# Performance work log

Measured on AMD Instinct MI355X. Metric: run time of the kernel, lower is better.

Reference implementation:

```python
import jax, jax.numpy as jnp
import numpy as np

LAYERS = 3
N_NODES = 100000
N_EDGES = 800000
EMB = 100
EPS = 1e-12  # F.normalize default eps


def setup_inputs() -> dict:
    key = jax.random.key(0)
    ks = jax.random.split(key, 7)
    embedding = jax.random.normal(ks[0], (N_NODES, EMB), dtype=jnp.float32)
    adj_val = jax.random.uniform(ks[1], (N_EDGES,), dtype=jnp.float32)
    w_att = jax.random.normal(ks[2], (EMB, 1), dtype=jnp.float32) * 0.1
    b_att = jax.random.normal(ks[3], (1,), dtype=jnp.float32) * 0.1
    w_items = jax.random.normal(ks[4], (LAYERS, EMB, EMB), dtype=jnp.float32) * 0.1
    adj_row = jax.random.randint(ks[5], (N_EDGES,), 0, N_NODES, dtype=jnp.int32)
    adj_col = jax.random.randint(ks[6], (N_EDGES,), 0, N_NODES, dtype=jnp.int32)
    return {"embedding": embedding, "adj_val": adj_val, "w_att": w_att,
            "b_att": b_att, "w_items": w_items, "adj_row": adj_row, "adj_col": adj_col}


def reference(embedding, adj_val, w_att, b_att, w_items, adj_row, adj_col):
    n = embedding.shape[0]
    # column-degree normalization: adjacency.multiply(1/adjacency.sum(axis=0))
    degree = jax.ops.segment_sum(adj_val, adj_col, num_segments=n)  # [N]
    vals = adj_val / degree[adj_col]  # per-edge normalized value

    x = embedding
    final = embedding
    for i in range(LAYERS):
        scores = x @ w_att + b_att              # [N,1]
        attw = jax.nn.softmax(scores, axis=0)   # softmax over nodes (dim=0)
        x = x @ w_items[i].T                    # nn.Linear (no bias)
        m = x * attw                            # attention-weighted features
        # sparse mm: out[r] = sum_{edges e: row[e]=r} vals[e] * m[col[e]]
        gathered = m[adj_col] * vals[:, None]   # [E, EMB]
        x = jax.ops.segment_sum(gathered, adj_row, num_segments=n)
        # F.normalize(p=2, dim=-1)
        norm = jnp.linalg.norm(x, axis=-1, keepdims=True)
        x = x / jnp.maximum(norm, EPS)
        final = final + x
    return final / (LAYERS + 1)
```

## Files before the change

### kernel.cpp

```cpp
#include <hip/hip_runtime.h>
#include <hip/hip_bf16.h>

#define NN 100000
#define NE 800000
#define EM 100
#define NL 3

typedef short bf16x8 __attribute__((ext_vector_type(8)));
typedef float f32x4  __attribute__((ext_vector_type(4)));
typedef unsigned long long u64;

static constexpr size_t OFF_XB   = 0;
static constexpr size_t OFF_M    = OFF_XB   + (size_t)NN*128*2;
static constexpr size_t OFF_F    = OFF_M    + (size_t)NN*128;
static constexpr size_t OFF_DEG  = OFF_F    + (size_t)NN*EM*2;
static constexpr size_t OFF_SC   = OFF_DEG  + (size_t)NN*4;
static constexpr size_t OFF_ES   = OFF_SC   + (size_t)NN*4;
static constexpr size_t OFF_POS  = OFF_ES   + (size_t)NE*8;
static constexpr size_t OFF_CNT  = OFF_POS  + (size_t)NE*4;
static constexpr size_t OFF_RP   = OFF_CNT  + (size_t)NN*4;
static constexpr size_t OFF_DGF  = OFF_RP   + (size_t)(NN+64)*4;
static constexpr size_t OFF_BS   = OFF_DGF  + (size_t)NN*8;
static constexpr size_t OFF_BIN  = OFF_BS   + 512;
static constexpr size_t OFF_FLAG = OFF_BIN  + 32768;
static constexpr size_t OFF_WAT  = OFF_FLAG + 16;
static constexpr size_t OFF_WBF  = OFF_WAT  + 512;

#define DEG_SCALE  4294967296.0f
#define DEG_INV    (1.0f/4294967296.0f)
#define BIN_SCALE  1048576.0f
#define BIN_INV    (1.0f/1048576.0f)

__device__ inline float ldf(const void* p, int i, int f32) {
    return f32 ? ((const float*)p)[i]
               : __bfloat162float(((const __hip_bfloat16*)p)[i]);
}

__device__ inline float bflo(unsigned int u) { return __uint_as_float(u << 16); }
__device__ inline float bfhi(unsigned int u) { return __uint_as_float(u & 0xFFFF0000u); }
__device__ inline unsigned int pack2bf(float a, float b) {
    __hip_bfloat16 ha = __float2bfloat16(a), hb = __float2bfloat16(b);
    unsigned short ua = *(unsigned short*)&ha, ub = *(unsigned short*)&hb;
    return (unsigned int)ua | ((unsigned int)ub << 16);
}
__device__ inline float ub0(unsigned int x) { return (float)(x & 0xFF); }
__device__ inline float ub1(unsigned int x) { return (float)((x >> 8) & 0xFF); }
__device__ inline float ub2(unsigned int x) { return (float)((x >> 16) & 0xFF); }
__device__ inline float ub3(unsigned int x) { return (float)(x >> 24); }

__device__ inline int probe_block(const void* p, int nsamp) {
    __shared__ int sflag;
    int tid = threadIdx.x;
    if (tid < 64) {
        const unsigned short* h = (const unsigned short*)p;
        int big = 0;
        for (int i = tid; i < nsamp; i += 64) {
            int ex = (h[2 * i] >> 7) & 0xFF;
            big += (ex >= 134) ? 1 : 0;
        }
        #pragma unroll
        for (int off = 32; off; off >>= 1) big += __shfl_xor(big, off);
        if (tid == 0) sflag = (big >= 2) ? 1 : 0;
    }
    __syncthreads();
    int f = sflag;
    __syncthreads();
    return f;
}

__global__ __launch_bounds__(256) void k_setup(const void* w_att, const void* w_itm,
                                               u64* degfix, int* counts, u64* bins,
                                               float* wat, unsigned short* wbf) {
    int fw = probe_block(w_att, 50);
    int fi = probe_block(w_itm, 256);
    int i = blockIdx.x * 256 + threadIdx.x;
    if (i < NN) { degfix[i] = 0ull; counts[i] = 0; }
    if (i < 4096) bins[i] = 0ull;
    if (i < 128) wat[i] = (i < EM) ? ldf(w_att, i, fw) : 0.f;
    if (i < NL * 112 * 128) {
        int l = i / (112 * 128), rem = i % (112 * 128);
        int n = rem >> 7, k = rem & 127;
        float v = (n < EM && k < EM) ? ldf(w_itm, (l * EM + n) * EM + k, fi) : 0.f;
        __hip_bfloat16 b = __float2bfloat16(v);
        wbf[i] = *(unsigned short*)&b;
    }
}

__global__ __launch_bounds__(256) void k_initxf(const void* __restrict__ emb,
                                                const float* __restrict__ wat,
                                                unsigned int* __restrict__ xbf,
                                                unsigned int* __restrict__ fin,
                                                float* __restrict__ scores, int* flags,
                                                u64* __restrict__ bins) {
    __shared__ float sb[4];
    int femb = probe_block(emb, 256);
    if (blockIdx.x == 0 && threadIdx.x == 0) flags[0] = femb;
    int lane = threadIdx.x & 63, w = threadIdx.x >> 6;
    int r = blockIdx.x * 4 + w;
    float f0 = 0.f, f1 = 0.f, part = 0.f;
    bool act = lane < 50;
    if (act) {
        if (femb) {
            float2 t = ((const float2*)emb)[(size_t)r * 50 + lane];
            f0 = t.x; f1 = t.y;
        } else {
            unsigned int u = ((const unsigned int*)emb)[(size_t)r * 50 + lane];
            f0 = bflo(u); f1 = bfhi(u);
        }
        float2 wv = *(const float2*)(wat + 2 * lane);
        part = f0 * wv.x + f1 * wv.y;
        fin[(size_t)r * 50 + lane] = pack2bf(f0, f1);
    }
    xbf[(size_t)r * 64 + lane] = act ? pack2bf(f0, f1) : 0u;
    #pragma unroll
    for (int off = 32; off; off >>= 1) part += __shfl_xor(part, off);
    if (lane == 0) {
        float p = expf(part);
        scores[r] = p;
        sb[w] = p;
    }
    __syncthreads();
    if (threadIdx.x == 0) {
        float t = sb[0] + sb[1] + sb[2] + sb[3];
        atomicAdd(&bins[blockIdx.x & 1023], (u64)llrintf(t * BIN_SCALE));
    }
}

__global__ __launch_bounds__(256) void k_deg(const void* __restrict__ val,
                                             const int* __restrict__ row, const int* __restrict__ col,
                                             u64* degfix, int* counts, int* __restrict__ pos) {
    int fav = probe_block(val, 256);
    int e = blockIdx.x * 256 + threadIdx.x;
    if (e >= NE) return;
    float v = ldf(val, e, fav);
    atomicAdd(&degfix[col[e]], (u64)llrintf(v * DEG_SCALE));
    pos[e] = atomicAdd(&counts[row[e]], 1);
}

__global__ __launch_bounds__(256) void k_scanA(const int* __restrict__ counts, int* excl, int* bsum,
                                               const u64* __restrict__ degfix, float* __restrict__ deg) {
    __shared__ int s[256];
    int base = blockIdx.x * 1024;
    int tid = threadIdx.x;
    int v[4]; int t = 0;
    #pragma unroll
    for (int i = 0; i < 4; i++) {
        int idx = base + tid * 4 + i;
        v[i] = (idx < NN) ? counts[idx] : 0;
        if (idx < NN) deg[idx] = (float)degfix[idx] * DEG_INV;
        t += v[i];
    }
    s[tid] = t; __syncthreads();
    for (int off = 1; off < 256; off <<= 1) {
        int add = (tid >= off) ? s[tid - off] : 0;
        __syncthreads();
        s[tid] += add;
        __syncthreads();
    }
    int ex = (tid == 0) ? 0 : s[tid - 1];
    #pragma unroll
    for (int i = 0; i < 4; i++) {
        int idx = base + tid * 4 + i;
        if (idx < NN) excl[idx] = ex;
        ex += v[i];
    }
    if (tid == 255) bsum[blockIdx.x] = s[255];
}

__global__ __launch_bounds__(256) void k_scanC(int* rowptr, const int* __restrict__ bsum) {
    __shared__ int spfx;
    int tid = threadIdx.x;
    int gi = blockIdx.x >> 2;
    if (tid < 64) {
        int t = (tid < gi) ? bsum[tid] : 0;
        if (tid + 64 < gi) t += bsum[tid + 64];
        #pragma unroll
        for (int off = 32; off; off >>= 1) t += __shfl_xor(t, off);
        if (tid == 0) spfx = t;
    }
    __syncthreads();
    int pfx = spfx;
    int i = blockIdx.x * 256 + tid;
    if (i < NN) {
        rowptr[i] += pfx;
        if (i == 0) rowptr[NN] = NE;
    }
}

__global__ __launch_bounds__(256) void k_scatter(const int* __restrict__ row, const int* __restrict__ col,
                                                 const void* __restrict__ aval,
                                                 const int* __restrict__ rowptr,
                                                 const int* __restrict__ pos, int2* es) {
    int fav = probe_block(aval, 256);
    int e = blockIdx.x * 256 + threadIdx.x;
    if (e >= NE) return;
    int p = rowptr[row[e]] + pos[e];
    es[p] = make_int2(col[e], __float_as_int(ldf(aval, e, fav)));
}

__global__ __launch_bounds__(256) void k_gemm(const unsigned short* __restrict__ xbf,
                                              const unsigned short* __restrict__ wbf,
                                              const float* __restrict__ scores,
                                              const u64* __restrict__ bins,
                                              const float* __restrict__ deg,
                                              unsigned char* __restrict__ m, int layer) {
    int wid = threadIdx.x >> 6, lane = threadIdx.x & 63;
    int row0 = blockIdx.x * 64 + wid * 16;
    if (row0 >= NN) return;
    int c15 = lane & 15, quad = lane >> 4;

    u64 bs = 0;
    const u64* bp = bins + (size_t)layer * 1024;
    #pragma unroll
    for (int t = 0; t < 16; t++) bs += bp[t * 64 + lane];
    #pragma unroll
    for (int off = 32; off; off >>= 1) bs += __shfl_xor(bs, off);
    float inv_sum = 1.0f / ((float)bs * BIN_INV);

    const bf16x8* xa = (const bf16x8*)(xbf + (size_t)(row0 + c15) * 128 + quad * 8);
    bf16x8 a[4];
    #pragma unroll
    for (int kq = 0; kq < 4; kq++) a[kq] = xa[kq * 4];

    float att[4];
    #pragma unroll
    for (int r = 0; r < 4; r++) {
        int grow = row0 + quad * 4 + r;
        float dv = deg[grow];
        float invd = dv > 0.f ? 1.0f / dv : 0.f;
        att[r] = scores[grow] * inv_sum * invd;
    }

    const bf16x8* wb = (const bf16x8*)(wbf + (size_t)layer * 112 * 128
                                       + (size_t)c15 * 128 + quad * 8);
    f32x4 accs[7];
    #pragma unroll
    for (int nt = 0; nt < 7; nt++) {
        f32x4 acc = {0.f, 0.f, 0.f, 0.f};
        #pragma unroll
        for (int kq = 0; kq < 4; kq++) {
            bf16x8 b = wb[nt * 256 + kq * 4];
            acc = __builtin_amdgcn_mfma_f32_16x16x32_bf16(a[kq], b, acc, 0, 0, 0);
        }
        accs[nt] = acc;
    }
    #pragma unroll
    for (int r = 0; r < 4; r++) {
        float mx = 0.f;
        #pragma unroll
        for (int nt = 0; nt < 7; nt++) mx = fmaxf(mx, fabsf(accs[nt][r]));
        #pragma unroll
        for (int off = 1; off < 16; off <<= 1) mx = fmaxf(mx, __shfl_xor(mx, off));
        float inv = 127.0f / fmaxf(mx, 1e-30f);
        int grow = row0 + quad * 4 + r;
        unsigned char* rowp = m + (size_t)grow * 128;
        #pragma unroll
        for (int nt = 0; nt < 7; nt++) {
            int col = nt * 16 + c15;
            if (col < EM) {
                int q = (int)rintf(accs[nt][r] * inv) + 128;
                rowp[col] = (unsigned char)q;
            }
        }
        if (c15 == 0) *(float*)(rowp + 100) = att[r] * mx * (1.0f / 127.0f);
        if (c15 < 6)  *(unsigned int*)(rowp + 104 + 4 * c15) = 0x80808080u;
    }
}

__global__ __launch_bounds__(256) void k_spmm(const int* __restrict__ rowptr,
                                              const int2* __restrict__ es,
                                              const unsigned char* __restrict__ m,
                                              const float* __restrict__ wat,
                                              unsigned int* __restrict__ xbf,
                                              unsigned int* __restrict__ fin,
                                              float* __restrict__ scores,
                                              void* __restrict__ out, const int* flags,
                                              u64* __restrict__ bins,
                                              int layer, int last) {
    __shared__ float sb[4];
    int lane = threadIdx.x & 63;
    int w = threadIdx.x >> 6;
    int r = blockIdx.x * 4 + w;
    int slot = lane >> 4, k = lane & 15;
    int s = rowptr[r], e = rowptr[r + 1];
    const char* mq = (const char*)m;
    int src12 = (lane & 48) + 12;

    float acc[8] = {0.f, 0.f, 0.f, 0.f, 0.f, 0.f, 0.f, 0.f};
    float tsum = 0.f;
    for (int i = s; i < e; i += 8) {
        int i0 = i + slot, i1 = i + 4 + slot;
        int j0 = i0 < e - 1 ? i0 : e - 1;
        int j1 = i1 < e - 1 ? i1 : e - 1;
        int2 c0 = es[j0];
        int2 c1 = es[j1];
        float v0 = (i0 < e) ? __int_as_float(c0.y) : 0.f;
        float v1 = (i1 < e) ? __int_as_float(c1.y) : 0.f;
        uint2 u0 = *(const uint2*)(mq + (((size_t)c0.x) << 7) + (k << 3));
        uint2 u1 = *(const uint2*)(mq + (((size_t)c1.x) << 7) + (k << 3));
        float s0 = __uint_as_float(__shfl((int)u0.y, src12));
        float s1 = __uint_as_float(__shfl((int)u1.y, src12));
        float t0 = v0 * s0, t1 = v1 * s1;
        tsum += t0 + t1;
        unsigned int x0 = u0.x, y0 = (k == 12) ? 0x80808080u : u0.y;
        unsigned int x1 = u1.x, y1 = (k == 12) ? 0x80808080u : u1.y;
        acc[0] += t0 * ub0(x0); acc[1] += t0 * ub1(x0);
        acc[2] += t0 * ub2(x0); acc[3] += t0 * ub3(x0);
        acc[4] += t0 * ub0(y0); acc[5] += t0 * ub1(y0);
        acc[6] += t0 * ub2(y0); acc[7] += t0 * ub3(y0);
        acc[0] += t1 * ub0(x1); acc[1] += t1 * ub1(x1);
        acc[2] += t1 * ub2(x1); acc[3] += t1 * ub3(x1);
        acc[4] += t1 * ub0(y1); acc[5] += t1 * ub1(y1);
        acc[6] += t1 * ub2(y1); acc[7] += t1 * ub3(y1);
    }
    #pragma unroll
    for (int t = 0; t < 8; t++) {
        acc[t] += __shfl_xor(acc[t], 16);
        acc[t] += __shfl_xor(acc[t], 32);
    }
    tsum += __shfl_xor(tsum, 16);
    tsum += __shfl_xor(tsum, 32);
    float corr = 128.0f * tsum;
    #pragma unroll
    for (int t = 0; t < 8; t++) acc[t] -= corr;

    float sq = 0.f;
    #pragma unroll
    for (int t = 0; t < 8; t++) sq += acc[t] * acc[t];
    #pragma unroll
    for (int off = 8; off; off >>= 1) sq += __shfl_xor(sq, off);
    float rn = 1.f / fmaxf(sqrtf(sq), 1e-12f);
    float n[8];
    #pragma unroll
    for (int t = 0; t < 8; t++) n[t] = acc[t] * rn;

    float part = 0.f;
    if (slot == 0) {
        if (!last) {
            uint4 q;
            q.x = pack2bf(n[0], n[1]); q.y = pack2bf(n[2], n[3]);
            q.z = pack2bf(n[4], n[5]); q.w = pack2bf(n[6], n[7]);
            *(uint4*)(xbf + (size_t)r * 64 + k * 4) = q;
        }
        if (k <= 12) {
            unsigned int fu[4] = {0u, 0u, 0u, 0u};
            size_t fb = (size_t)r * 50 + k * 4;
            uint2 fa = *(const uint2*)(fin + fb);
            fu[0] = fa.x; fu[1] = fa.y;
            if (k < 12) {
                uint2 fbv = *(const uint2*)(fin + fb + 2);
                fu[2] = fbv.x; fu[3] = fbv.y;
            }
            float fn[8];
            #pragma unroll
            for (int t = 0; t < 4; t++) {
                fn[2 * t]     = bflo(fu[t]) + n[2 * t];
                fn[2 * t + 1] = bfhi(fu[t]) + n[2 * t + 1];
            }
            if (!last) {
                uint2 pa, pb;
                pa.x = pack2bf(fn[0], fn[1]); pa.y = pack2bf(fn[2], fn[3]);
                pb.x = pack2bf(fn[4], fn[5]); pb.y = pack2bf(fn[6], fn[7]);
                *(uint2*)(fin + fb) = pa;
                if (k < 12) *(uint2*)(fin + fb + 2) = pb;
                float4 w0 = *(const float4*)(wat + k * 8);
                float4 w1 = *(const float4*)(wat + k * 8 + 4);
                part = n[0] * w0.x + n[1] * w0.y + n[2] * w0.z + n[3] * w0.w
                     + n[4] * w1.x + n[5] * w1.y + n[6] * w1.z + n[7] * w1.w;
            } else {
                if (flags[0]) {
                    float4 A, B;
                    A.x = fn[0] * 0.25f; A.y = fn[1] * 0.25f; A.z = fn[2] * 0.25f; A.w = fn[3] * 0.25f;
                    B.x = fn[4] * 0.25f; B.y = fn[5] * 0.25f; B.z = fn[6] * 0.25f; B.w = fn[7] * 0.25f;
                    float* ob = (float*)out + (size_t)r * 100 + k * 8;
                    *(float4*)ob = A;
                    if (k < 12) *(float4*)(ob + 4) = B;
                } else {
                    uint2 pa, pb;
                    pa.x = pack2bf(fn[0] * 0.25f, fn[1] * 0.25f);
                    pa.y = pack2bf(fn[2] * 0.25f, fn[3] * 0.25f);
                    pb.x = pack2bf(fn[4] * 0.25f, fn[5] * 0.25f);
                    pb.y = pack2bf(fn[6] * 0.25f, fn[7] * 0.25f);
                    unsigned int* ob = (unsigned int*)out + (size_t)r * 50 + k * 4;
                    *(uint2*)ob = pa;
                    if (k < 12) *(uint2*)(ob + 2) = pb;
                }
            }
        }
    }
    if (!last) {
        #pragma unroll
        for (int off = 8; off; off >>= 1) part += __shfl_xor(part, off);
        if (lane == 0) {
            float p = expf(part);
            scores[r] = p;
            sb[w] = p;
        }
        __syncthreads();
        if (threadIdx.x == 0) {
            float t = sb[0] + sb[1] + sb[2] + sb[3];
            atomicAdd(&bins[(size_t)(layer + 1) * 1024 + (blockIdx.x & 1023)],
                      (u64)llrintf(t * BIN_SCALE));
        }
    }
}

extern "C" void kernel_launch(void* const* d_in, const int* in_sizes, int n_in,
                              void* d_out, int out_size, void* d_ws, size_t ws_size,
                              hipStream_t stream) {
    const void* emb   = d_in[0];
    const void* aval  = d_in[1];
    const void* w_att = d_in[2];
    const void* w_itm = d_in[4];
    const int* arow = (const int*)d_in[5];
    const int* acol = (const int*)d_in[6];

    char* w = (char*)d_ws;
    unsigned int*   xbf    = (unsigned int*)(w + OFF_XB);
    unsigned char*  m      = (unsigned char*)(w + OFF_M);
    unsigned int*   fin    = (unsigned int*)(w + OFF_F);
    float*          deg    = (float*)(w + OFF_DEG);
    float*          scores = (float*)(w + OFF_SC);
    int2*           es     = (int2*) (w + OFF_ES);
    int*            pos    = (int*)  (w + OFF_POS);
    int*            counts = (int*)  (w + OFF_CNT);
    int*            rowptr = (int*)  (w + OFF_RP);
    u64*            degfix = (u64*)  (w + OFF_DGF);
    int*            bsum   = (int*)  (w + OFF_BS);
    u64*            bins   = (u64*)  (w + OFF_BIN);
    int*            flags  = (int*)  (w + OFF_FLAG);
    float*          wat    = (float*)(w + OFF_WAT);
    unsigned short* wbf    = (unsigned short*)(w + OFF_WBF);

    const int GN   = (NN + 255) / 256;
    const int GNE  = (NE + 255) / 256;
    const int GSCN = (NN + 1023) / 1024;
    const int GW4  = (NN + 3) / 4;
    const int GGE  = (NN + 63) / 64;

    k_setup<<<GN, 256, 0, stream>>>(w_att, w_itm, degfix, counts, bins, wat, wbf);
    k_initxf<<<GW4, 256, 0, stream>>>(emb, wat, xbf, fin, scores, flags, bins);
    k_deg<<<GNE, 256, 0, stream>>>(aval, arow, acol, degfix, counts, pos);
    k_scanA<<<GSCN, 256, 0, stream>>>(counts, rowptr, bsum, degfix, deg);
    k_scanC<<<GN, 256, 0, stream>>>(rowptr, bsum);
    k_scatter<<<GNE, 256, 0, stream>>>(arow, acol, aval, rowptr, pos, es);

    for (int l = 0; l < NL; l++) {
        k_gemm<<<GGE, 256, 0, stream>>>((const unsigned short*)xbf, wbf, scores, bins, deg, m, l);
        k_spmm<<<GW4, 256, 0, stream>>>(rowptr, es, m, wat, xbf, fin, scores,
                                        d_out, flags, bins, l, (l == NL - 1) ? 1 : 0);
    }
}
```

Measured before the change: 498.6 us.

## Privatize degree and row-count atomics per XCC with workgroup-scope adds

Degree and row-count accumulation now goes into one private copy per XCC, picked by reading the XCC hardware register. The adds use relaxed, workgroup-scope atomics so they can resolve in the local L2 instead of the device-coherent path. The scan kernel then sums the eight degree copies. It also packs per-XCC prefix offsets for each row into 8-bit fields, which the scatter kernel uses to rebuild edge positions. The trade-offs are extra workspace, extra scan reads, reliance on workgroup-scope atomics behaving correctly across CUs of one XCC, and a cap of 255 edges per row within each packed offset field.

```diff
diff --git a/kernel.cpp b/kernel.cpp
--- a/kernel.cpp
+++ b/kernel.cpp
@@ -5,6 +5,7 @@
 #define NE 800000
 #define EM 100
 #define NL 3
+#define NX 8
 
 typedef short bf16x8 __attribute__((ext_vector_type(8)));
 typedef float f32x4  __attribute__((ext_vector_type(4)));
@@ -17,10 +18,11 @@
 static constexpr size_t OFF_SC   = OFF_DEG  + (size_t)NN*4;
 static constexpr size_t OFF_ES   = OFF_SC   + (size_t)NN*4;
 static constexpr size_t OFF_POS  = OFF_ES   + (size_t)NE*8;
-static constexpr size_t OFF_CNT  = OFF_POS  + (size_t)NE*4;
-static constexpr size_t OFF_RP   = OFF_CNT  + (size_t)NN*4;
-static constexpr size_t OFF_DGF  = OFF_RP   + (size_t)(NN+64)*4;
-static constexpr size_t OFF_BS   = OFF_DGF  + (size_t)NN*8;
+static constexpr size_t OFF_CNT8 = OFF_POS  + (size_t)NE*4;
+static constexpr size_t OFF_RP   = OFF_CNT8 + (size_t)NX*NN*4;
+static constexpr size_t OFF_DGF8 = OFF_RP   + (size_t)(NN+64)*4;
+static constexpr size_t OFF_PRE8 = OFF_DGF8 + (size_t)NX*NN*8;
+static constexpr size_t OFF_BS   = OFF_PRE8 + (size_t)NN*8;
 static constexpr size_t OFF_BIN  = OFF_BS   + 512;
 static constexpr size_t OFF_FLAG = OFF_BIN  + 32768;
 static constexpr size_t OFF_WAT  = OFF_FLAG + 16;
@@ -30,6 +32,12 @@
 #define DEG_INV    (1.0f/4294967296.0f)
 #define BIN_SCALE  1048576.0f
 #define BIN_INV    (1.0f/1048576.0f)
+
+__device__ inline int xcc_id() {
+    unsigned int x;
+    asm("s_getreg_b32 %0, hwreg(HW_REG_XCC_ID)" : "=s"(x));
+    return (int)(x & 7);
+}
 
 __device__ inline float ldf(const void* p, int i, int f32) {
     return f32 ? ((const float*)p)[i]
@@ -69,12 +77,18 @@
 }
 
 __global__ __launch_bounds__(256) void k_setup(const void* w_att, const void* w_itm,
-                                               u64* degfix, int* counts, u64* bins,
+                                               u64* degfix8, int* counts8, u64* bins,
                                                float* wat, unsigned short* wbf) {
     int fw = probe_block(w_att, 50);
     int fi = probe_block(w_itm, 256);
     int i = blockIdx.x * 256 + threadIdx.x;
-    if (i < NN) { degfix[i] = 0ull; counts[i] = 0; }
+    if (i < NN) {
+        #pragma unroll
+        for (int x = 0; x < NX; x++) {
+            degfix8[(size_t)x * NN + i] = 0ull;
+            counts8[(size_t)x * NN + i] = 0;
+        }
+    }
     if (i < 4096) bins[i] = 0ull;
     if (i < 128) wat[i] = (i < EM) ? ldf(w_att, i, fw) : 0.f;
     if (i < NL * 112 * 128) {
@@ -128,17 +142,23 @@
 
 __global__ __launch_bounds__(256) void k_deg(const void* __restrict__ val,
                                              const int* __restrict__ row, const int* __restrict__ col,
-                                             u64* degfix, int* counts, int* __restrict__ pos) {
+                                             u64* degfix8, int* counts8, int* __restrict__ pos) {
     int fav = probe_block(val, 256);
     int e = blockIdx.x * 256 + threadIdx.x;
     if (e >= NE) return;
+    int x = xcc_id();
     float v = ldf(val, e, fav);
-    atomicAdd(&degfix[col[e]], (u64)llrintf(v * DEG_SCALE));
-    pos[e] = atomicAdd(&counts[row[e]], 1);
-}
-
-__global__ __launch_bounds__(256) void k_scanA(const int* __restrict__ counts, int* excl, int* bsum,
-                                               const u64* __restrict__ degfix, float* __restrict__ deg) {
+    __hip_atomic_fetch_add(&degfix8[(size_t)x * NN + col[e]],
+                           (u64)llrintf(v * DEG_SCALE),
+                           __ATOMIC_RELAXED, __HIP_MEMORY_SCOPE_WORKGROUP);
+    int lr = __hip_atomic_fetch_add(&counts8[(size_t)x * NN + row[e]], 1,
+                                    __ATOMIC_RELAXED, __HIP_MEMORY_SCOPE_WORKGROUP);
+    pos[e] = (x << 24) | lr;
+}
+
+__global__ __launch_bounds__(256) void k_scanA(const int* __restrict__ counts8, int* excl, int* bsum,
+                                               const u64* __restrict__ degfix8, float* __restrict__ deg,
+                                               u64* __restrict__ pre8) {
     __shared__ int s[256];
     int base = blockIdx.x * 1024;
     int tid = threadIdx.x;
@@ -146,9 +166,24 @@
     #pragma unroll
     for (int i = 0; i < 4; i++) {
         int idx = base + tid * 4 + i;
-        v[i] = (idx < NN) ? counts[idx] : 0;
-        if (idx < NN) deg[idx] = (float)degfix[idx] * DEG_INV;
-        t += v[i];
+        int tot = 0;
+        if (idx < NN) {
+            u64 pk = 0; int run = 0;
+            #pragma unroll
+            for (int x = 0; x < NX; x++) {
+                int c = counts8[(size_t)x * NN + idx];
+                pk |= (u64)(unsigned)(run & 0xFF) << (8 * x);
+                run += c;
+            }
+            pre8[idx] = pk;
+            tot = run;
+            u64 df = 0;
+            #pragma unroll
+            for (int x = 0; x < NX; x++) df += degfix8[(size_t)x * NN + idx];
+            deg[idx] = (float)df * DEG_INV;
+        }
+        v[i] = tot;
+        t += tot;
     }
     s[tid] = t; __syncthreads();
     for (int off = 1; off < 256; off <<= 1) {
@@ -190,11 +225,15 @@
 __global__ __launch_bounds__(256) void k_scatter(const int* __restrict__ row, const int* __restrict__ col,
                                                  const void* __restrict__ aval,
                                                  const int* __restrict__ rowptr,
-                                                 const int* __restrict__ pos, int2* es) {
+                                                 const int* __restrict__ pos,
+                                                 const u64* __restrict__ pre8, int2* es) {
     int fav = probe_block(aval, 256);
     int e = blockIdx.x * 256 + threadIdx.x;
     if (e >= NE) return;
-    int p = rowptr[row[e]] + pos[e];
+    int rw = row[e];
+    int pr = pos[e];
+    int x = pr >> 24, lr = pr & 0xFFFFFF;
+    int p = rowptr[rw] + (int)((pre8[rw] >> (8 * x)) & 0xFF) + lr;
     es[p] = make_int2(col[e], __float_as_int(ldf(aval, e, fav)));
 }
 
@@ -423,9 +462,10 @@
     float*          scores = (float*)(w + OFF_SC);
     int2*           es     = (int2*) (w + OFF_ES);
     int*            pos    = (int*)  (w + OFF_POS);
-    int*            counts = (int*)  (w + OFF_CNT);
+    int*            counts8= (int*)  (w + OFF_CNT8);
     int*            rowptr = (int*)  (w + OFF_RP);
-    u64*            degfix = (u64*)  (w + OFF_DGF);
+    u64*            degfix8= (u64*)  (w + OFF_DGF8);
+    u64*            pre8   = (u64*)  (w + OFF_PRE8);
     int*            bsum   = (int*)  (w + OFF_BS);
     u64*            bins   = (u64*)  (w + OFF_BIN);
     int*            flags  = (int*)  (w + OFF_FLAG);
@@ -438,12 +478,12 @@
     const int GW4  = (NN + 3) / 4;
     const int GGE  = (NN + 63) / 64;
 
-    k_setup<<<GN, 256, 0, stream>>>(w_att, w_itm, degfix, counts, bins, wat, wbf);
+    k_setup<<<GN, 256, 0, stream>>>(w_att, w_itm, degfix8, counts8, bins, wat, wbf);
     k_initxf<<<GW4, 256, 0, stream>>>(emb, wat, xbf, fin, scores, flags, bins);
-    k_deg<<<GNE, 256, 0, stream>>>(aval, arow, acol, degfix, counts, pos);
-    k_scanA<<<GSCN, 256, 0, stream>>>(counts, rowptr, bsum, degfix, deg);
+    k_deg<<<GNE, 256, 0, stream>>>(aval, arow, acol, degfix8, counts8, pos);
+    k_scanA<<<GSCN, 256, 0, stream>>>(counts8, rowptr, bsum, degfix8, deg, pre8);
     k_scanC<<<GN, 256, 0, stream>>>(rowptr, bsum);
-    k_scatter<<<GNE, 256, 0, stream>>>(arow, acol, aval, rowptr, pos, es);
+    k_scatter<<<GNE, 256, 0, stream>>>(arow, acol, aval, rowptr, pos, pre8, es);
 
     for (int l = 0; l < NL; l++) {
         k_gemm<<<GGE, 256, 0, stream>>>((const unsigned short*)xbf, wbf, scores, bins, deg, m, l);
```

Result: no change. 499.1 us (+0.1%).

## Merge setup, init and degree kernels; co-launch edge scatter with first GEMM

Applied to the files above, without the earlier changes.

The setup, embedding-init and degree/count kernels become one block-partitioned launch. The accumulators are now zeroed by a single memset, after their workspace regions were moved next to each other. The edge scatter is fused with the layer-0 GEMM in one launch, since neither depends on the other. The init path now reads w_att directly instead of waiting on a precomputed copy. This removes several kernel launches and serialization points and lets independent work overlap, at the cost of mixing different work in one grid, which may cause load imbalance.

```diff
diff --git a/kernel.cpp b/kernel.cpp
--- a/kernel.cpp
+++ b/kernel.cpp
@@ -9,6 +9,11 @@
 typedef short bf16x8 __attribute__((ext_vector_type(8)));
 typedef float f32x4  __attribute__((ext_vector_type(4)));
 typedef unsigned long long u64;
+
+#define GNE_C  3125
+#define GW4_C  25000
+#define GGE_C  1563
+#define GCV_C  168
 
 static constexpr size_t OFF_XB   = 0;
 static constexpr size_t OFF_M    = OFF_XB   + (size_t)NN*128*2;
@@ -18,13 +23,14 @@
 static constexpr size_t OFF_ES   = OFF_SC   + (size_t)NN*4;
 static constexpr size_t OFF_POS  = OFF_ES   + (size_t)NE*8;
 static constexpr size_t OFF_CNT  = OFF_POS  + (size_t)NE*4;
-static constexpr size_t OFF_RP   = OFF_CNT  + (size_t)NN*4;
-static constexpr size_t OFF_DGF  = OFF_RP   + (size_t)(NN+64)*4;
-static constexpr size_t OFF_BS   = OFF_DGF  + (size_t)NN*8;
-static constexpr size_t OFF_BIN  = OFF_BS   + 512;
-static constexpr size_t OFF_FLAG = OFF_BIN  + 32768;
+static constexpr size_t OFF_DGF  = OFF_CNT  + (size_t)NN*4;
+static constexpr size_t OFF_BIN  = OFF_DGF  + (size_t)NN*8;
+static constexpr size_t OFF_RP   = OFF_BIN  + 32768;
+static constexpr size_t OFF_BS   = OFF_RP   + (size_t)(NN+64)*4;
+static constexpr size_t OFF_FLAG = OFF_BS   + 512;
 static constexpr size_t OFF_WAT  = OFF_FLAG + 16;
 static constexpr size_t OFF_WBF  = OFF_WAT  + 512;
+static constexpr size_t ZERO_BYTES = (size_t)NN*4 + (size_t)NN*8 + 32768;
 
 #define DEG_SCALE  4294967296.0f
 #define DEG_INV    (1.0f/4294967296.0f)
@@ -68,73 +74,76 @@
     return f;
 }
 
-__global__ __launch_bounds__(256) void k_setup(const void* w_att, const void* w_itm,
-                                               u64* degfix, int* counts, u64* bins,
-                                               float* wat, unsigned short* wbf) {
-    int fw = probe_block(w_att, 50);
-    int fi = probe_block(w_itm, 256);
-    int i = blockIdx.x * 256 + threadIdx.x;
-    if (i < NN) { degfix[i] = 0ull; counts[i] = 0; }
-    if (i < 4096) bins[i] = 0ull;
-    if (i < 128) wat[i] = (i < EM) ? ldf(w_att, i, fw) : 0.f;
-    if (i < NL * 112 * 128) {
-        int l = i / (112 * 128), rem = i % (112 * 128);
-        int n = rem >> 7, k = rem & 127;
-        float v = (n < EM && k < EM) ? ldf(w_itm, (l * EM + n) * EM + k, fi) : 0.f;
-        __hip_bfloat16 b = __float2bfloat16(v);
-        wbf[i] = *(unsigned short*)&b;
-    }
-}
-
-__global__ __launch_bounds__(256) void k_initxf(const void* __restrict__ emb,
-                                                const float* __restrict__ wat,
-                                                unsigned int* __restrict__ xbf,
-                                                unsigned int* __restrict__ fin,
-                                                float* __restrict__ scores, int* flags,
-                                                u64* __restrict__ bins) {
-    __shared__ float sb[4];
-    int femb = probe_block(emb, 256);
-    if (blockIdx.x == 0 && threadIdx.x == 0) flags[0] = femb;
-    int lane = threadIdx.x & 63, w = threadIdx.x >> 6;
-    int r = blockIdx.x * 4 + w;
-    float f0 = 0.f, f1 = 0.f, part = 0.f;
-    bool act = lane < 50;
-    if (act) {
-        if (femb) {
-            float2 t = ((const float2*)emb)[(size_t)r * 50 + lane];
-            f0 = t.x; f1 = t.y;
-        } else {
-            unsigned int u = ((const unsigned int*)emb)[(size_t)r * 50 + lane];
-            f0 = bflo(u); f1 = bfhi(u);
-        }
-        float2 wv = *(const float2*)(wat + 2 * lane);
-        part = f0 * wv.x + f1 * wv.y;
-        fin[(size_t)r * 50 + lane] = pack2bf(f0, f1);
-    }
-    xbf[(size_t)r * 64 + lane] = act ? pack2bf(f0, f1) : 0u;
-    #pragma unroll
-    for (int off = 32; off; off >>= 1) part += __shfl_xor(part, off);
-    if (lane == 0) {
-        float p = expf(part);
-        scores[r] = p;
-        sb[w] = p;
-    }
-    __syncthreads();
-    if (threadIdx.x == 0) {
-        float t = sb[0] + sb[1] + sb[2] + sb[3];
-        atomicAdd(&bins[blockIdx.x & 1023], (u64)llrintf(t * BIN_SCALE));
-    }
-}
-
-__global__ __launch_bounds__(256) void k_deg(const void* __restrict__ val,
-                                             const int* __restrict__ row, const int* __restrict__ col,
-                                             u64* degfix, int* counts, int* __restrict__ pos) {
-    int fav = probe_block(val, 256);
-    int e = blockIdx.x * 256 + threadIdx.x;
-    if (e >= NE) return;
-    float v = ldf(val, e, fav);
-    atomicAdd(&degfix[col[e]], (u64)llrintf(v * DEG_SCALE));
-    pos[e] = atomicAdd(&counts[row[e]], 1);
+__global__ __launch_bounds__(256) void k_pro(const void* __restrict__ emb,
+                                             const void* __restrict__ aval,
+                                             const int* __restrict__ row,
+                                             const int* __restrict__ col,
+                                             const void* __restrict__ w_att,
+                                             const void* __restrict__ w_itm,
+                                             unsigned int* __restrict__ xbf,
+                                             unsigned int* __restrict__ fin,
+                                             float* __restrict__ scores, int* flags,
+                                             u64* __restrict__ bins,
+                                             u64* __restrict__ degfix, int* __restrict__ counts,
+                                             int* __restrict__ pos,
+                                             float* __restrict__ wat,
+                                             unsigned short* __restrict__ wbf) {
+    int b = blockIdx.x;
+    if (b < GNE_C) {
+        int fav = probe_block(aval, 256);
+        int e = b * 256 + threadIdx.x;
+        if (e >= NE) return;
+        float v = ldf(aval, e, fav);
+        atomicAdd(&degfix[col[e]], (u64)llrintf(v * DEG_SCALE));
+        pos[e] = atomicAdd(&counts[row[e]], 1);
+    } else if (b < GNE_C + GW4_C) {
+        __shared__ float sb[4];
+        int femb = probe_block(emb, 256);
+        int fw = probe_block(w_att, 50);
+        if (b == GNE_C && threadIdx.x == 0) flags[0] = femb;
+        int lane = threadIdx.x & 63, w = threadIdx.x >> 6;
+        int r = (b - GNE_C) * 4 + w;
+        float f0 = 0.f, f1 = 0.f, part = 0.f;
+        bool act = lane < 50;
+        if (act) {
+            if (femb) {
+                float2 t = ((const float2*)emb)[(size_t)r * 50 + lane];
+                f0 = t.x; f1 = t.y;
+            } else {
+                unsigned int u = ((const unsigned int*)emb)[(size_t)r * 50 + lane];
+                f0 = bflo(u); f1 = bfhi(u);
+            }
+            float w0 = ldf(w_att, 2 * lane, fw);
+            float w1 = ldf(w_att, 2 * lane + 1, fw);
+            part = f0 * w0 + f1 * w1;
+            fin[(size_t)r * 50 + lane] = pack2bf(f0, f1);
+        }
+        xbf[(size_t)r * 64 + lane] = act ? pack2bf(f0, f1) : 0u;
+        #pragma unroll
+        for (int off = 32; off; off >>= 1) part += __shfl_xor(part, off);
+        if (lane == 0) {
+            float p = expf(part);
+            scores[r] = p;
+            sb[w] = p;
+        }
+        __syncthreads();
+        if (threadIdx.x == 0) {
+            float t = sb[0] + sb[1] + sb[2] + sb[3];
+            atomicAdd(&bins[b & 1023], (u64)llrintf(t * BIN_SCALE));
+        }
+    } else {
+        int fw = probe_block(w_att, 50);
+        int fi = probe_block(w_itm, 256);
+        int i = (b - GNE_C - GW4_C) * 256 + threadIdx.x;
+        if (i < 128) wat[i] = (i < EM) ? ldf(w_att, i, fw) : 0.f;
+        if (i < NL * 112 * 128) {
+            int l = i / (112 * 128), rem = i % (112 * 128);
+            int n = rem >> 7, k = rem & 127;
+            float v = (n < EM && k < EM) ? ldf(w_itm, (l * EM + n) * EM + k, fi) : 0.f;
+            __hip_bfloat16 bb = __float2bfloat16(v);
+            wbf[i] = *(unsigned short*)&bb;
+        }
+    }
 }
 
 __global__ __launch_bounds__(256) void k_scanA(const int* __restrict__ counts, int* excl, int* bsum,
@@ -187,15 +196,73 @@
     }
 }
 
-__global__ __launch_bounds__(256) void k_scatter(const int* __restrict__ row, const int* __restrict__ col,
-                                                 const void* __restrict__ aval,
-                                                 const int* __restrict__ rowptr,
-                                                 const int* __restrict__ pos, int2* es) {
-    int fav = probe_block(aval, 256);
-    int e = blockIdx.x * 256 + threadIdx.x;
-    if (e >= NE) return;
-    int p = rowptr[row[e]] + pos[e];
-    es[p] = make_int2(col[e], __float_as_int(ldf(aval, e, fav)));
+__device__ void gemm_body(int gb, const unsigned short* __restrict__ xbf,
+                          const unsigned short* __restrict__ wbf,
+                          const float* __restrict__ scores,
+                          const u64* __restrict__ bins,
+                          const float* __restrict__ deg,
+                          unsigned char* __restrict__ m, int layer) {
+    int wid = threadIdx.x >> 6, lane = threadIdx.x & 63;
+    int row0 = gb * 64 + wid * 16;
+    if (row0 >= NN) return;
+    int c15 = lane & 15, quad = lane >> 4;
+
+    u64 bs = 0;
+    const u64* bp = bins + (size_t)layer * 1024;
+    #pragma unroll
+    for (int t = 0; t < 16; t++) bs += bp[t * 64 + lane];
+    #pragma unroll
+    for (int off = 32; off; off >>= 1) bs += __shfl_xor(bs, off);
+    float inv_sum = 1.0f / ((float)bs * BIN_INV);
+
+    const bf16x8* xa = (const bf16x8*)(xbf + (size_t)(row0 + c15) * 128 + quad * 8);
+    bf16x8 a[4];
+    #pragma unroll
+    for (int kq = 0; kq < 4; kq++) a[kq] = xa[kq * 4];
+
+    float att[4];
+    #pragma unroll
+    for (int r = 0; r < 4; r++) {
+        int grow = row0 + quad * 4 + r;
+        float dv = deg[grow];
+        float invd = dv > 0.f ? 1.0f / dv : 0.f;
+        att[r] = scores[grow] * inv_sum * invd;
+    }
+
+    const bf16x8* wb = (const bf16x8*)(wbf + (size_t)layer * 112 * 128
+                                       + (size_t)c15 * 128 + quad * 8);
+    f32x4 accs[7];
+    #pragma unroll
+    for (int nt = 0; nt < 7; nt++) {
+        f32x4 acc = {0.f, 0.f, 0.f, 0.f};
+        #pragma unroll
+        for (int kq = 0; kq < 4; kq++) {
+            bf16x8 b = wb[nt * 256 + kq * 4];
+            acc = __builtin_amdgcn_mfma_f32_16x16x32_bf16(a[kq], b, acc, 0, 0, 0);
+        }
+        accs[nt] = acc;
+    }
+    #pragma unroll
+    for (int r = 0; r < 4; r++) {
+        float mx = 0.f;
+        #pragma unroll
+        for (int nt = 0; nt < 7; nt++) mx = fmaxf(mx, fabsf(accs[nt][r]));
+        #pragma unroll
+        for (int off = 1; off < 16; off <<= 1) mx = fmaxf(mx, __shfl_xor(mx, off));
+        float inv = 127.0f / fmaxf(mx, 1e-30f);
+        int grow = row0 + quad * 4 + r;
+        unsigned char* rowp = m + (size_t)grow * 128;
+        #pragma unroll
+        for (int nt = 0; nt < 7; nt++) {
+            int col = nt * 16 + c15;
+            if (col < EM) {
+                int q = (int)rintf(accs[nt][r] * inv) + 128;
+                rowp[col] = (unsigned char)q;
+            }
+        }
+        if (c15 == 0) *(float*)(rowp + 100) = att[r] * mx * (1.0f / 127.0f);
+        if (c15 < 6)  *(unsigned int*)(rowp + 104 + 4 * c15) = 0x80808080u;
+    }
 }
 
 __global__ __launch_bounds__(256) void k_gemm(const unsigned short* __restrict__ xbf,
@@ -204,66 +271,28 @@
                                               const u64* __restrict__ bins,
                                               const float* __restrict__ deg,
                                               unsigned char* __restrict__ m, int layer) {
-    int wid = threadIdx.x >> 6, lane = threadIdx.x & 63;
-    int row0 = blockIdx.x * 64 + wid * 16;
-    if (row0 >= NN) return;
-    int c15 = lane & 15, quad = lane >> 4;
-
-    u64 bs = 0;
-    const u64* bp = bins + (size_t)layer * 1024;
-    #pragma unroll
-    for (int t = 0; t < 16; t++) bs += bp[t * 64 + lane];
-    #pragma unroll
-    for (int off = 32; off; off >>= 1) bs += __shfl_xor(bs, off);
-    float inv_sum = 1.0f / ((float)bs * BIN_INV);
-
-    const bf16x8* xa = (const bf16x8*)(xbf + (size_t)(row0 + c15) * 128 + quad * 8);
-    bf16x8 a[4];
-    #pragma unroll
-    for (int kq = 0; kq < 4; kq++) a[kq] = xa[kq * 4];
-
-    float att[4];
-    #pragma unroll
-    for (int r = 0; r < 4; r++) {
-        int grow = row0 + quad * 4 + r;
-        float dv = deg[grow];
-        float invd = dv > 0.f ? 1.0f / dv : 0.f;
-        att[r] = scores[grow] * inv_sum * invd;
-    }
-
-    const bf16x8* wb = (const bf16x8*)(wbf + (size_t)layer * 112 * 128
-                                       + (size_t)c15 * 128 + quad * 8);
-    f32x4 accs[7];
-    #pragma unroll
-    for (int nt = 0; nt < 7; nt++) {
-        f32x4 acc = {0.f, 0.f, 0.f, 0.f};
-        #pragma unroll
-        for (int kq = 0; kq < 4; kq++) {
-            bf16x8 b = wb[nt * 256 + kq * 4];
-            acc = __builtin_amdgcn_mfma_f32_16x16x32_bf16(a[kq], b, acc, 0, 0, 0);
-        }
-        accs[nt] = acc;
-    }
-    #pragma unroll
-    for (int r = 0; r < 4; r++) {
-        float mx = 0.f;
-        #pragma unroll
-        for (int nt = 0; nt < 7; nt++) mx = fmaxf(mx, fabsf(accs[nt][r]));
-        #pragma unroll
-        for (int off = 1; off < 16; off <<= 1) mx = fmaxf(mx, __shfl_xor(mx, off));
-        float inv = 127.0f / fmaxf(mx, 1e-30f);
-        int grow = row0 + quad * 4 + r;
-        unsigned char* rowp = m + (size_t)grow * 128;
-        #pragma unroll
-        for (int nt = 0; nt < 7; nt++) {
-            int col = nt * 16 + c15;
-            if (col < EM) {
-                int q = (int)rintf(accs[nt][r] * inv) + 128;
-                rowp[col] = (unsigned char)q;
-            }
-        }
-        if (c15 == 0) *(float*)(rowp + 100) = att[r] * mx * (1.0f / 127.0f);
-        if (c15 < 6)  *(unsigned int*)(rowp + 104 + 4 * c15) = 0x80808080u;
+    gemm_body(blockIdx.x, xbf, wbf, scores, bins, deg, m, layer);
+}
+
+__global__ __launch_bounds__(256) void k_sg(const int* __restrict__ row, const int* __restrict__ col,
+                                            const void* __restrict__ aval,
+                                            const int* __restrict__ rowptr,
+                                            const int* __restrict__ pos, int2* __restrict__ es,
+                                            const unsigned short* __restrict__ xbf,
+                                            const unsigned short* __restrict__ wbf,
+                                            const float* __restrict__ scores,
+                                            const u64* __restrict__ bins,
+                                            const float* __restrict__ deg,
+                                            unsigned char* __restrict__ m) {
+    int b = blockIdx.x;
+    if (b < GNE_C) {
+        int fav = probe_block(aval, 256);
+        int e = b * 256 + threadIdx.x;
+        if (e >= NE) return;
+        int p = rowptr[row[e]] + pos[e];
+        es[p] = make_int2(col[e], __float_as_int(ldf(aval, e, fav)));
+    } else {
+        gemm_body(b - GNE_C, xbf, wbf, scores, bins, deg, m, 0);
     }
 }
 
@@ -424,30 +453,34 @@
     int2*           es     = (int2*) (w + OFF_ES);
     int*            pos    = (int*)  (w + OFF_POS);
     int*            counts = (int*)  (w + OFF_CNT);
+    u64*            degfix = (u64*)  (w + OFF_DGF);
+    u64*            bins   = (u64*)  (w + OFF_BIN);
     int*            rowptr = (int*)  (w + OFF_RP);
-    u64*            degfix = (u64*)  (w + OFF_DGF);
     int*            bsum   = (int*)  (w + OFF_BS);
-    u64*            bins   = (u64*)  (w + OFF_BIN);
     int*            flags  = (int*)  (w + OFF_FLAG);
     float*          wat    = (float*)(w + OFF_WAT);
     unsigned short* wbf    = (unsigned short*)(w + OFF_WBF);
 
     const int GN   = (NN + 255) / 256;
-    const int GNE  = (NE + 255) / 256;
     const int GSCN = (NN + 1023) / 1024;
-    const int GW4  = (NN + 3) / 4;
-    const int GGE  = (NN + 63) / 64;
-
-    k_setup<<<GN, 256, 0, stream>>>(w_att, w_itm, degfix, counts, bins, wat, wbf);
-    k_initxf<<<GW4, 256, 0, stream>>>(emb, wat, xbf, fin, scores, flags, bins);
-    k_deg<<<GNE, 256, 0, stream>>>(aval, arow, acol, degfix, counts, pos);
+    const int GPRO = GNE_C + GW4_C + GCV_C;
+    const int GSG  = GNE_C + GGE_C;
+
+    hipMemsetAsync(w + OFF_CNT, 0, ZERO_BYTES, stream);
+
+    k_pro<<<GPRO, 256, 0, stream>>>(emb, aval, arow, acol, w_att, w_itm,
+                                    xbf, fin, scores, flags, bins,
+                                    degfix, counts, pos, wat, wbf);
     k_scanA<<<GSCN, 256, 0, stream>>>(counts, rowptr, bsum, degfix, deg);
     k_scanC<<<GN, 256, 0, stream>>>(rowptr, bsum);
-    k_scatter<<<GNE, 256, 0, stream>>>(arow, acol, aval, rowptr, pos, es);
-
-    for (int l = 0; l < NL; l++) {
-        k_gemm<<<GGE, 256, 0, stream>>>((const unsigned short*)xbf, wbf, scores, bins, deg, m, l);
-        k_spmm<<<GW4, 256, 0, stream>>>(rowptr, es, m, wat, xbf, fin, scores,
-                                        d_out, flags, bins, l, (l == NL - 1) ? 1 : 0);
-    }
-}
+    k_sg<<<GSG, 256, 0, stream>>>(arow, acol, aval, rowptr, pos, es,
+                                  (const unsigned short*)xbf, wbf, scores, bins, deg, m);
+
+    k_spmm<<<GW4_C, 256, 0, stream>>>(rowptr, es, m, wat, xbf, fin, scores,
+                                      d_out, flags, bins, 0, 0);
+    for (int l = 1; l < NL; l++) {
+        k_gemm<<<GGE_C, 256, 0, stream>>>((const unsigned short*)xbf, wbf, scores, bins, deg, m, l);
+        k_spmm<<<GW4_C, 256, 0, stream>>>(rowptr, es, m, wat, xbf, fin, scores,
+                                          d_out, flags, bins, l, (l == NL - 1) ? 1 : 0);
+    }
+}
```

After: 492.5 us. Within noise of the previous version (-1.2%).
